# Kernel optimization log

Measured on AMD Instinct MI355X. Metric: run time of the kernel, lower is better.

Reference implementation:

```python
import jax, jax.numpy as jnp
import numpy as np

G = 8          # deformable groups
K = 9          # 3x3 kernel points
MAXR = 10.0    # max_residue_magnitude


def conv2d(x, w, b):
    # x: [B,Cin,H,W], w: [Cout,Cin,3,3], SAME padding, stride 1
    y = jax.lax.conv_general_dilated(x, w, (1, 1), ((1, 1), (1, 1)),
                                     dimension_numbers=('NCHW', 'OIHW', 'NCHW'))
    return y + b[None, :, None, None]


def lrelu(x):
    return jnp.where(x >= 0, x, 0.1 * x)


def offset_branch(x, ws, bs):
    for w, b in zip(ws[:-1], bs[:-1]):
        x = lrelu(conv2d(x, w, b))
    return conv2d(x, ws[-1], bs[-1])


def mdcn(x, offset, mask, w, b):
    # Modulated deformable conv, 3x3, stride 1, pad 1, dilation 1, groups=1.
    # offset: [B, G*K*2, H, W] ordered (g, k, (y,x)); mask: [B, G*K, H, W]
    B, C, H, W = x.shape
    Cg = C // G
    off = offset.reshape(B, G, K, 2, H, W)
    m = mask.reshape(B, G, K, H, W)
    ky = (jnp.arange(K) // 3 - 1).astype(x.dtype)   # kernel dy, pad=1
    kx = (jnp.arange(K) % 3 - 1).astype(x.dtype)    # kernel dx
    hy = jnp.arange(H, dtype=x.dtype)
    wx = jnp.arange(W, dtype=x.dtype)
    py = hy[None, None, None, :, None] + ky[None, None, :, None, None] + off[:, :, :, 0]  # [B,G,K,H,W]
    px = wx[None, None, None, None, :] + kx[None, None, :, None, None] + off[:, :, :, 1]
    y0f = jnp.floor(py); x0f = jnp.floor(px)
    ly = py - y0f; lx = px - x0f
    y0 = y0f.astype(jnp.int32); x0 = x0f.astype(jnp.int32)
    xf = x.reshape(B, G, Cg, H * W)

    def gather(yi, xi):
        valid = ((yi >= 0) & (yi < H) & (xi >= 0) & (xi < W)).astype(x.dtype)
        yc = jnp.clip(yi, 0, H - 1)
        xc = jnp.clip(xi, 0, W - 1)
        idx = (yc * W + xc).reshape(B, G, 1, K * H * W)
        v = jnp.take_along_axis(xf, idx, axis=3).reshape(B, G, Cg, K, H, W)
        return v * valid.reshape(B, G, 1, K, H, W)

    ly_ = ly[:, :, None]; lx_ = lx[:, :, None]  # [B,G,1,K,H,W]
    samp = (gather(y0, x0) * (1 - ly_) * (1 - lx_)
            + gather(y0, x0 + 1) * (1 - ly_) * lx_
            + gather(y0 + 1, x0) * ly_ * (1 - lx_)
            + gather(y0 + 1, x0 + 1) * ly_ * lx_)
    samp = samp * m[:, :, None]                 # modulation
    wr = w.reshape(w.shape[0], G, Cg, K)        # [Cout,G,Cg,K]
    return jnp.einsum('ogck,bgckhw->bohw', wr, samp) + b[None, :, None, None]


def setup_inputs():
    key = jax.random.key(0)
    ks = jax.random.split(key, 40)
    B, C, H, W = 1, 64, 256, 256
    s = 0.05
    inp = {
        'feat_prev': jax.random.normal(ks[0], (B, C, H, W), jnp.float32),
        'feat_next': jax.random.normal(ks[1], (B, C, H, W), jnp.float32),
        'extra_feat_prev': jax.random.normal(ks[2], (B, 2 * C, H, W), jnp.float32),
        'extra_feat_next': jax.random.normal(ks[3], (B, 2 * C, H, W), jnp.float32),
        'flow_prev': jax.random.normal(ks[4], (B, 2, H, W), jnp.float32),
        'flow_next': jax.random.normal(ks[5], (B, 2, H, W), jnp.float32),
    }
    shapes = [(C, 2 * C, 3, 3), (C, C, 3, 3), (C, C, 3, 3), (27 * G, C, 3, 3)]
    i = 6
    for pre in ('off1', 'off2'):
        for j, sh in enumerate(shapes):
            inp[f'{pre}_w{j}'] = jax.random.normal(ks[i], sh, jnp.float32) * s; i += 1
            inp[f'{pre}_b{j}'] = jax.random.normal(ks[i], (sh[0],), jnp.float32) * s; i += 1
    inp['dcn1_w'] = jax.random.normal(ks[i], (C, C, 3, 3), jnp.float32) * s; i += 1
    inp['dcn1_b'] = jax.random.normal(ks[i], (C,), jnp.float32) * s; i += 1
    inp['dcn2_w'] = jax.random.normal(ks[i], (C, C, 3, 3), jnp.float32) * s; i += 1
    inp['dcn2_b'] = jax.random.normal(ks[i], (C,), jnp.float32) * s; i += 1
    inp['fus_w'] = jax.random.normal(ks[i], (C, 2 * C, 3, 3), jnp.float32) * s; i += 1
    inp['fus_b'] = jax.random.normal(ks[i], (C,), jnp.float32) * s
    return inp


def reference(feat_prev, feat_next, extra_feat_prev, extra_feat_next, flow_prev, flow_next,
              off1_w0, off1_b0, off1_w1, off1_b1, off1_w2, off1_b2, off1_w3, off1_b3,
              off2_w0, off2_b0, off2_w1, off2_b1, off2_w2, off2_b2, off2_w3, off2_b3,
              dcn1_w, dcn1_b, dcn2_w, dcn2_b, fus_w, fus_b):
    def branch(feat, extra, flow, ws, bs, dw, db):
        out = offset_branch(extra, ws, bs)
        o1, o2, msk = jnp.split(out, 3, axis=1)
        off = MAXR * jnp.tanh(jnp.concatenate([o1, o2], axis=1))
        off = off + jnp.tile(flow[:, ::-1], (1, off.shape[1] // 2, 1, 1))  # flip(1).repeat
        msk = jax.nn.sigmoid(msk)
        return mdcn(feat, off, msk, dw, db)

    fp = branch(feat_prev, extra_feat_prev, flow_prev,
                [off1_w0, off1_w1, off1_w2, off1_w3], [off1_b0, off1_b1, off1_b2, off1_b3],
                dcn1_w, dcn1_b)
    fn = branch(feat_next, extra_feat_next, flow_next,
                [off2_w0, off2_w1, off2_w2, off2_w3], [off2_b0, off2_b1, off2_b2, off2_b3],
                dcn2_w, dcn2_b)
    return conv2d(jnp.concatenate([fp, fn], axis=1), fus_w, fus_b)
```

## Files before the change

### kernel.cpp

```cpp
#include <hip/hip_runtime.h>
#include <cstddef>
#include <cstdint>

constexpr int IMG = 256;
constexpr int NPIX = 65536;
constexpr int PW = 258;
constexpr size_t PREC = (size_t)PW * PW;

typedef _Float16 h8 __attribute__((ext_vector_type(8)));
typedef float f32x4 __attribute__((ext_vector_type(4)));

template<int CIN>
__device__ __forceinline__ void zero_pad_rec(int i, _Float16* buf)
{
  constexpr int Q = CIN / 8;
  if (i >= 1028 * Q) return;
  int pr = i / Q, qi = i - pr * Q;
  int rec;
  if (pr < 258) rec = pr;
  else if (pr < 516) rec = 257 * 258 + (pr - 258);
  else { int j = pr - 516; rec = (1 + (j >> 1)) * 258 + ((j & 1) ? 257 : 0); }
  *reinterpret_cast<uint4*>(&buf[(size_t)rec * CIN + qi * 8]) = uint4{0, 0, 0, 0};
}

template<int CIN>
__global__ __launch_bounds__(256) void zeropad_k(_Float16* __restrict__ buf)
{
  zero_pad_rec<CIN>(blockIdx.x * 256 + threadIdx.x, buf);
}

template<int CIN>
__global__ __launch_bounds__(256) void prep_hwc_k(
    const float* __restrict__ in, _Float16* __restrict__ out)
{
  int b = blockIdx.x;
  if (b >= 256) { zero_pad_rec<CIN>((b - 256) * 256 + threadIdx.x, out); return; }
  int pix = b * 256 + threadIdx.x;
  int py = pix >> 8, px = pix & 255;
  size_t rec = ((size_t)(py + 1) * PW + px + 1) * CIN;
#pragma unroll
  for (int c0 = 0; c0 < CIN; c0 += 8) {
    _Float16 t[8];
#pragma unroll
    for (int j = 0; j < 8; ++j)
      t[j] = (_Float16)in[(size_t)(c0 + j) * NPIX + pix];
    *reinterpret_cast<uint4*>(&out[rec + c0]) = *reinterpret_cast<uint4*>(t);
  }
}

__device__ __forceinline__ void wfrag(
    const float* __restrict__ w, int cin_tot, int cin_off, int KC, int NBF,
    int nvalid, int idx, _Float16* __restrict__ oHi, _Float16* __restrict__ oLo)
{
  int l = idx & 63;
  int r = idx >> 6;
  int fg = r % NBF; r /= NBF;
  int c = r % KC;
  int t = r / KC;
  int n = fg * 16 + (l & 15);
  int cinb = c * 32 + (l >> 4) * 8;
  _Float16 vh[8], vl[8];
#pragma unroll
  for (int j = 0; j < 8; ++j) {
    float x = 0.f;
    if (n < nvalid) x = w[((size_t)n * cin_tot + cin_off + cinb + j) * 9 + t];
    vh[j] = (_Float16)x;
    vl[j] = (_Float16)(x - (float)vh[j]);
  }
  *reinterpret_cast<uint4*>(oHi + (size_t)idx * 8) = *reinterpret_cast<uint4*>(vh);
  if (oLo)
    *reinterpret_cast<uint4*>(oLo + (size_t)idx * 8) = *reinterpret_cast<uint4*>(vl);
}

__global__ __launch_bounds__(256) void wprep_all_k(
    const float* __restrict__ w0, const float* __restrict__ w1,
    const float* __restrict__ w2, const float* __restrict__ w3,
    const float* __restrict__ wf, int wf_cin_off, const float* __restrict__ dw,
    _Float16* b0h, _Float16* b0l, _Float16* b1h, _Float16* b1l,
    _Float16* b2h, _Float16* b2l, _Float16* b3h, _Float16* b3l,
    _Float16* bfh, _Float16* __restrict__ wB)
{
  int idx = blockIdx.x * 256 + threadIdx.x;
  if (idx < 9216)       wfrag(w0, 128, 0, 4, 4, 64, idx, b0h, b0l);
  else if (idx < 13824) wfrag(w1, 64, 0, 2, 4, 64, idx - 9216, b1h, b1l);
  else if (idx < 18432) wfrag(w2, 64, 0, 2, 4, 64, idx - 13824, b2h, b2l);
  else if (idx < 36864) wfrag(w3, 64, 0, 2, 16, 216, idx - 18432, b3h, b3l);
  else if (idx < 41472) wfrag(wf, 128, wf_cin_off, 2, 4, 64, idx - 36864, bfh, nullptr);
  else if (idx < 46080) {
    int i = idx - 41472;
    int l = i & 63;
    int r = i >> 6;
    int f = r & 3;
    int p = r >> 2;
    int t = p * 4 + (l >> 4);
    int g = (t * 57) >> 9;
    int k = t - 9 * g;
    int n = f * 16 + (l & 15);
    _Float16 v[8];
#pragma unroll
    for (int j = 0; j < 8; ++j)
      v[j] = (_Float16)dw[(size_t)n * 576 + g * 72 + j * 9 + k];
    *reinterpret_cast<uint4*>(wB + (size_t)i * 8) = *reinterpret_cast<uint4*>(v);
  }
}

template<int CIN, int EPI, bool DBL, typename OT>
__global__ __launch_bounds__(256) void conv_mfma_k(
    const _Float16* __restrict__ act, const _Float16* __restrict__ wHi,
    const _Float16* __restrict__ wLo, const float* __restrict__ bias,
    OT* __restrict__ out, int ncout, int NBF)
{
  constexpr int Q = CIN / 8;
  constexpr int KC = CIN / 32;
  constexpr int NT = DBL ? 2 : 1;
  constexpr int NREC = 198;
  __shared__ __align__(16) _Float16 sA[NREC * CIN];

  const int tid = threadIdx.x;
  const int lane = tid & 63;
  const int wv = tid >> 6;
  const int b = blockIdx.x;
  const int inner = b >> 3;
  const int y = (b & 7) * 32 + (inner & 31);
  const int x0 = (inner >> 5) << 6;
  const int n0 = blockIdx.y << 6;

  for (int i = tid; i < NREC * Q; i += 256) {
    int rec = i / Q, q = i - rec * Q;
    int seg = rec / 66, xr = rec - seg * 66;
    size_t g = ((size_t)(y + seg) * PW + x0 + xr) * CIN + q * 8;
    int slot = (q + rec) & (Q - 1);
    *reinterpret_cast<uint4*>(&sA[rec * CIN + slot * 8]) =
        *reinterpret_cast<const uint4*>(&act[g]);
  }

  const int fgb = (n0 >> 4) + wv;
  auto bload = [&](int t, int c, const _Float16* src) {
    return *reinterpret_cast<const h8*>(
        &src[((((size_t)t * KC + c) * NBF + fgb) * 64 + lane) * 8]);
  };
  h8 Bn[KC][NT];
#pragma unroll
  for (int c = 0; c < KC; ++c) {
    Bn[c][0] = bload(0, c, wHi);
    if (DBL) Bn[c][1] = bload(0, c, wLo);
  }

  f32x4 acc[4];
#pragma unroll
  for (int a = 0; a < 4; ++a) acc[a] = f32x4{0.f, 0.f, 0.f, 0.f};
  __syncthreads();

  const int m = lane & 15, kq = lane >> 4;
#pragma unroll 1
  for (int t = 0; t < 9; ++t) {
    h8 Bc[KC][NT];
#pragma unroll
    for (int c = 0; c < KC; ++c) {
      Bc[c][0] = Bn[c][0];
      if (DBL) Bc[c][1] = Bn[c][1];
    }
    if (t < 8) {
#pragma unroll
      for (int c = 0; c < KC; ++c) {
        Bn[c][0] = bload(t + 1, c, wHi);
        if (DBL) Bn[c][1] = bload(t + 1, c, wLo);
      }
    }
    const int lrb = (t / 3) * 66 + (t % 3) + m;
#pragma unroll
    for (int c = 0; c < KC; ++c) {
      const int q = c * 4 + kq;
#pragma unroll
      for (int mf = 0; mf < 4; ++mf) {
        int lr = lrb + mf * 16;
        int slot = (q + lr) & (Q - 1);
        h8 ah = *reinterpret_cast<const h8*>(&sA[lr * CIN + slot * 8]);
        acc[mf] = __builtin_amdgcn_mfma_f32_16x16x32_f16(
            ah, Bc[c][0], acc[mf], 0, 0, 0);
        if (DBL)
          acc[mf] = __builtin_amdgcn_mfma_f32_16x16x32_f16(
              ah, Bc[c][1], acc[mf], 0, 0, 0);
      }
    }
  }

  if (EPI == 0) {
    const int ch = wv * 16 + m;
    const float bv = bias[ch];
#pragma unroll
    for (int mf = 0; mf < 4; ++mf)
#pragma unroll
      for (int r = 0; r < 4; ++r) {
        int p = mf * 16 + kq * 4 + r;
        float v = acc[mf][r] + bv;
        v = (v >= 0.f) ? v : 0.1f * v;
        reinterpret_cast<_Float16*>(out)[((size_t)(y + 1) * PW + x0 + p + 1) * 64 + ch] =
            (_Float16)v;
      }
  } else {
    __syncthreads();
    float* sF = reinterpret_cast<float*>(sA);
    const int nl = wv * 16 + m;
#pragma unroll
    for (int mf = 0; mf < 4; ++mf) {
      int ml = mf * 16 + kq * 4;
      f32x4 v = acc[mf];
      if (EPI == 1) {
        float bv = (n0 + nl < ncout) ? bias[n0 + nl] : 0.f;
        v[0] += bv; v[1] += bv; v[2] += bv; v[3] += bv;
      }
      *reinterpret_cast<f32x4*>(&sF[nl * 68 + ml]) = v;
    }
    __syncthreads();
    for (int i = tid; i < 1024; i += 256) {
      int row = i >> 4, cx = (i & 15) * 4;
      int gc = n0 + row;
      if (gc < ncout) {
        f32x4 v = *reinterpret_cast<f32x4*>(&sF[row * 68 + cx]);
        size_t ob = (size_t)gc * NPIX + (size_t)y * IMG + x0 + cx;
        if (EPI == 2) {
          float* op = reinterpret_cast<float*>(out) + ob;
          op[0] += v[0]; op[1] += v[1]; op[2] += v[2]; op[3] += v[3];
        } else if (sizeof(OT) == 2) {
          _Float16 t4[4] = {(_Float16)v[0], (_Float16)v[1],
                            (_Float16)v[2], (_Float16)v[3]};
          *reinterpret_cast<uint2*>(reinterpret_cast<_Float16*>(out) + ob) =
              *reinterpret_cast<uint2*>(t4);
        } else {
          *reinterpret_cast<f32x4*>(reinterpret_cast<float*>(out) + ob) = v;
        }
      }
    }
  }
}

__global__ __launch_bounds__(256) void featg_k(
    const float* __restrict__ in, _Float16* __restrict__ out)
{
  int pix = blockIdx.x * 256 + threadIdx.x;
#pragma unroll
  for (int g = 0; g < 8; ++g) {
    _Float16 t[8];
#pragma unroll
    for (int c = 0; c < 8; ++c)
      t[c] = (_Float16)in[(size_t)(g * 8 + c) * NPIX + pix];
    *reinterpret_cast<uint4*>(&out[((size_t)g * NPIX + pix) * 8]) =
        *reinterpret_cast<uint4*>(t);
  }
}

struct GS {
  h8 a, b, c, d;
  _Float16 w00, w01, w10, w11;
  float r0, r1, r2;
  h8 bf0, bf1, bf2, bf3;
};

__global__ __launch_bounds__(256, 4) void mdcn_mfma_k(
    const _Float16* __restrict__ featG, const _Float16* __restrict__ o216,
    const float* __restrict__ flow, const _Float16* __restrict__ wB,
    const float* __restrict__ bias, _Float16* __restrict__ actF)
{
  const int tid = threadIdx.x;
  const int lane = tid & 63;
  const int wv = tid >> 6;
  const int b = blockIdx.x;
  const int inner = b >> 3;
  const int row = (b & 7) * 32 + (inner & 31);
  const int xseg = inner >> 5;
  const int m = lane & 15;
  const int tq = lane >> 4;
  const int xw = xseg * 64 + wv * 16;
  const int x = xw + m;
  const int pix = row * 256 + x;

  const float fy = flow[NPIX + pix];
  const float fx = flow[pix];
  const float rowf = (float)row, xf = (float)x;

  f32x4 acc[4];
#pragma unroll
  for (int f = 0; f < 4; ++f) acc[f] = f32x4{0.f, 0.f, 0.f, 0.f};

  auto rawloadv = [&](int p, float& a0, float& a1, float& a2) {
    int t = p * 4 + tq;
    int g = (t * 57) >> 9;
    int k = t - 9 * g;
    a0 = (float)o216[(size_t)(g * 18 + 2 * k) * NPIX + pix];
    a1 = (float)o216[(size_t)(g * 18 + 2 * k + 1) * NPIX + pix];
    a2 = (float)o216[(size_t)(144 + g * 9 + k) * NPIX + pix];
  };

  auto setup = [&](int p, float s0, float s1, float s2, GS& o) {
    const int t = p * 4 + tq;
    const int g = (t * 57) >> 9;
    const int k = t - 9 * g;
    const int kd = (k * 11) >> 5;
    const int km = k - 3 * kd;
    const float mm = __builtin_amdgcn_rcpf(1.f + __expf(-s2));
    const float e0 = __expf(2.f * s0);
    const float e1 = __expf(2.f * s1);
    const float th0 = 1.f - 2.f * __builtin_amdgcn_rcpf(e0 + 1.f);
    const float th1 = 1.f - 2.f * __builtin_amdgcn_rcpf(e1 + 1.f);
    const float pyf = rowf + (float)(kd - 1) + 10.f * th0 + fy;
    const float pxf = xf + (float)(km - 1) + 10.f * th1 + fx;
    const float y0f = floorf(pyf), x0f = floorf(pxf);
    const float ly = pyf - y0f, lx = pxf - x0f;
    const int y0 = (int)y0f, x0i = (int)x0f;
    const int y1 = y0 + 1, x1 = x0i + 1;
    const bool vy0 = (unsigned)y0 < (unsigned)IMG, vy1 = (unsigned)y1 < (unsigned)IMG;
    const bool vx0 = (unsigned)x0i < (unsigned)IMG, vx1 = (unsigned)x1 < (unsigned)IMG;
    const int y0c = min(max(y0, 0), IMG - 1), y1c = min(max(y1, 0), IMG - 1);
    const int x0c = min(max(x0i, 0), IMG - 1), x1c = min(max(x1, 0), IMG - 1);
    const float oy = 1.f - ly, ox = 1.f - lx;
    const float py0 = oy * mm, py1 = ly * mm;
    const float w00 = (vy0 && vx0) ? py0 * ox : 0.f;
    const float w01 = (vy0 && vx1) ? py0 * lx : 0.f;
    const float w10 = (vy1 && vx0) ? py1 * ox : 0.f;
    const float w11 = (vy1 && vx1) ? py1 * lx : 0.f;
    o.w00 = (_Float16)w00; o.w01 = (_Float16)w01;
    o.w10 = (_Float16)w10; o.w11 = (_Float16)w11;
    const _Float16* fg = featG + ((size_t)g << 19);
    o.a = *reinterpret_cast<const h8*>(fg + (size_t)(y0c * IMG + x0c) * 8);
    o.b = *reinterpret_cast<const h8*>(fg + (size_t)(y0c * IMG + x1c) * 8);
    o.c = *reinterpret_cast<const h8*>(fg + (size_t)(y1c * IMG + x0c) * 8);
    o.d = *reinterpret_cast<const h8*>(fg + (size_t)(y1c * IMG + x1c) * 8);
  };

  auto bfload = [&](int p, GS& o) {
    const _Float16* wp = wB + ((size_t)p * 256 + lane) * 8;
    o.bf0 = *reinterpret_cast<const h8*>(wp);
    o.bf1 = *reinterpret_cast<const h8*>(wp + 512);
    o.bf2 = *reinterpret_cast<const h8*>(wp + 1024);
    o.bf3 = *reinterpret_cast<const h8*>(wp + 1536);
  };

  auto consume = [&](GS& cur) {
    h8 af;
#pragma unroll
    for (int j = 0; j < 8; ++j)
      af[j] = (_Float16)(cur.a[j] * cur.w00 + cur.b[j] * cur.w01 +
                         cur.c[j] * cur.w10 + cur.d[j] * cur.w11);
    acc[0] = __builtin_amdgcn_mfma_f32_16x16x32_f16(af, cur.bf0, acc[0], 0, 0, 0);
    acc[1] = __builtin_amdgcn_mfma_f32_16x16x32_f16(af, cur.bf1, acc[1], 0, 0, 0);
    acc[2] = __builtin_amdgcn_mfma_f32_16x16x32_f16(af, cur.bf2, acc[2], 0, 0, 0);
    acc[3] = __builtin_amdgcn_mfma_f32_16x16x32_f16(af, cur.bf3, acc[3], 0, 0, 0);
  };

  auto body = [&](int p, GS& cur, GS& nxt) {
    setup(p + 1, nxt.r0, nxt.r1, nxt.r2, nxt);
    rawloadv(p + 2, cur.r0, cur.r1, cur.r2);
    bfload(p + 1, nxt);
    consume(cur);
  };

  GS A, B;
  {
    float t0, t1, t2;
    rawloadv(0, t0, t1, t2);
    rawloadv(1, B.r0, B.r1, B.r2);
    bfload(0, A);
    setup(0, t0, t1, t2, A);
  }

#pragma unroll 1
  for (int it = 0; it < 8; ++it) {
    body(2 * it, A, B);
    body(2 * it + 1, B, A);
  }
  setup(17, B.r0, B.r1, B.r2, B);
  bfload(17, B);
  consume(A);
  consume(B);

  const size_t rb = ((size_t)(row + 1) * PW + xw + 1) * 64;
#pragma unroll
  for (int f = 0; f < 4; ++f) {
    const int ch = f * 16 + m;
    const float bv = bias[ch];
#pragma unroll
    for (int r = 0; r < 4; ++r)
      actF[rb + (size_t)(tq * 4 + r) * 64 + ch] = (_Float16)(acc[f][r] + bv);
  }
}

extern "C" void kernel_launch(void* const* d_in, const int* in_sizes, int n_in,
                              void* d_out, int out_size, void* d_ws, size_t ws_size,
                              hipStream_t stream)
{
  const float* feat[2]  = {(const float*)d_in[0], (const float*)d_in[1]};
  const float* extra[2] = {(const float*)d_in[2], (const float*)d_in[3]};
  const float* flow[2]  = {(const float*)d_in[4], (const float*)d_in[5]};
  const float* ow[2][4];
  const float* ob[2][4];
  for (int br = 0; br < 2; ++br)
    for (int j = 0; j < 4; ++j) {
      ow[br][j] = (const float*)d_in[6 + br * 8 + j * 2];
      ob[br][j] = (const float*)d_in[6 + br * 8 + j * 2 + 1];
    }
  const float* dcnw[2] = {(const float*)d_in[22], (const float*)d_in[24]};
  const float* dcnb[2] = {(const float*)d_in[23], (const float*)d_in[25]};
  const float* fusw = (const float*)d_in[26];
  const float* fusb = (const float*)d_in[27];

  char* wsb = (char*)d_ws;
  size_t off = 0;
  auto alloc = [&](size_t bytes) {
    void* p = wsb + off;
    off += (bytes + 255) & ~(size_t)255;
    return p;
  };
  _Float16* actI = (_Float16*)alloc(PREC * 128 * 2);
  _Float16* actA = (_Float16*)alloc(PREC * 64 * 2);
  _Float16* actB = (_Float16*)alloc(PREC * 64 * 2);
  _Float16* actF = (_Float16*)alloc(PREC * 64 * 2);
  _Float16* o216 = (_Float16*)alloc((size_t)216 * NPIX * 2);
  _Float16* featG = (_Float16*)alloc((size_t)8 * NPIX * 8 * 2);
  _Float16* wB = (_Float16*)alloc(36864 * 2);
  _Float16* wb0h = (_Float16*)alloc(147456); _Float16* wb0l = (_Float16*)alloc(147456);
  _Float16* wb1h = (_Float16*)alloc(73728);  _Float16* wb1l = (_Float16*)alloc(73728);
  _Float16* wb2h = (_Float16*)alloc(73728);  _Float16* wb2l = (_Float16*)alloc(73728);
  _Float16* wb3h = (_Float16*)alloc(294912); _Float16* wb3l = (_Float16*)alloc(294912);
  _Float16* wbFh = (_Float16*)alloc(73728);
  float* outp = (float*)d_out;

  dim3 blk256(256);
  zeropad_k<64><<<dim3(33), blk256, 0, stream>>>(actA);
  zeropad_k<64><<<dim3(33), blk256, 0, stream>>>(actB);
  zeropad_k<64><<<dim3(33), blk256, 0, stream>>>(actF);

  for (int br = 0; br < 2; ++br) {
    prep_hwc_k<128><<<dim3(321), blk256, 0, stream>>>(extra[br], actI);
    wprep_all_k<<<dim3(180), blk256, 0, stream>>>(
        ow[br][0], ow[br][1], ow[br][2], ow[br][3], fusw, br * 64, dcnw[br],
        wb0h, wb0l, wb1h, wb1l, wb2h, wb2l, wb3h, wb3l, wbFh, wB);

    conv_mfma_k<128, 0, true, _Float16><<<dim3(1024, 1), blk256, 0, stream>>>(
        actI, wb0h, wb0l, ob[br][0], actA, 64, 4);
    conv_mfma_k<64, 0, true, _Float16><<<dim3(1024, 1), blk256, 0, stream>>>(
        actA, wb1h, wb1l, ob[br][1], actB, 64, 4);
    conv_mfma_k<64, 0, true, _Float16><<<dim3(1024, 1), blk256, 0, stream>>>(
        actB, wb2h, wb2l, ob[br][2], actA, 64, 4);
    conv_mfma_k<64, 1, true, _Float16><<<dim3(1024, 4), blk256, 0, stream>>>(
        actA, wb3h, wb3l, ob[br][3], o216, 216, 16);

    featg_k<<<dim3(256), blk256, 0, stream>>>(feat[br], featG);
    mdcn_mfma_k<<<dim3(1024), blk256, 0, stream>>>(
        featG, o216, flow[br], wB, dcnb[br], actF);

    if (br == 0)
      conv_mfma_k<64, 1, false, float><<<dim3(1024, 1), blk256, 0, stream>>>(
          actF, wbFh, nullptr, fusb, outp, 64, 4);
    else
      conv_mfma_k<64, 2, false, float><<<dim3(1024, 1), blk256, 0, stream>>>(
          actF, wbFh, nullptr, nullptr, outp, 64, 4);
  }
}
```

Measured before the change: 515.8 us.

## Batch both branches into single launches and fuse final conv over concatenated channels

Runs the previous and next branches together in every stage by using blockIdx.z to pick per-branch pointers, which halves the launch count and doubles the grid of each kernel. The deformable conv outputs of both branches are written interleaved into one 128-channel padded buffer, so the fusion conv runs once with CIN=128 instead of twice with a read-modify-write accumulate. Workspace buffers are aliased across stages to limit the extra memory. In exchange the working set per kernel doubles, and correctness now depends on the aliasing order and the zero padding of the reused buffers.

```diff
diff --git a/kernel.cpp b/kernel.cpp
--- a/kernel.cpp
+++ b/kernel.cpp
@@ -31,8 +31,12 @@
 
 template<int CIN>
 __global__ __launch_bounds__(256) void prep_hwc_k(
-    const float* __restrict__ in, _Float16* __restrict__ out)
-{
+    const float* __restrict__ in0, const float* __restrict__ in1,
+    _Float16* __restrict__ out0, _Float16* __restrict__ out1)
+{
+  const int z = blockIdx.z;
+  const float* in = z ? in1 : in0;
+  _Float16* out = z ? out1 : out0;
   int b = blockIdx.x;
   if (b >= 256) { zero_pad_rec<CIN>((b - 256) * 256 + threadIdx.x, out); return; }
   int pix = b * 256 + threadIdx.x;
@@ -75,7 +79,7 @@
 __global__ __launch_bounds__(256) void wprep_all_k(
     const float* __restrict__ w0, const float* __restrict__ w1,
     const float* __restrict__ w2, const float* __restrict__ w3,
-    const float* __restrict__ wf, int wf_cin_off, const float* __restrict__ dw,
+    const float* __restrict__ wf, const float* __restrict__ dw,
     _Float16* b0h, _Float16* b0l, _Float16* b1h, _Float16* b1l,
     _Float16* b2h, _Float16* b2l, _Float16* b3h, _Float16* b3l,
     _Float16* bfh, _Float16* __restrict__ wB)
@@ -85,9 +89,8 @@
   else if (idx < 13824) wfrag(w1, 64, 0, 2, 4, 64, idx - 9216, b1h, b1l);
   else if (idx < 18432) wfrag(w2, 64, 0, 2, 4, 64, idx - 13824, b2h, b2l);
   else if (idx < 36864) wfrag(w3, 64, 0, 2, 16, 216, idx - 18432, b3h, b3l);
-  else if (idx < 41472) wfrag(wf, 128, wf_cin_off, 2, 4, 64, idx - 36864, bfh, nullptr);
-  else if (idx < 46080) {
-    int i = idx - 41472;
+  else if (idx < 41472) {
+    int i = idx - 36864;
     int l = i & 63;
     int r = i >> 6;
     int f = r & 3;
@@ -102,19 +105,30 @@
       v[j] = (_Float16)dw[(size_t)n * 576 + g * 72 + j * 9 + k];
     *reinterpret_cast<uint4*>(wB + (size_t)i * 8) = *reinterpret_cast<uint4*>(v);
   }
+  else if (wf && idx < 50688)
+    wfrag(wf, 128, 0, 4, 4, 64, idx - 41472, bfh, nullptr);
 }
 
 template<int CIN, int EPI, bool DBL, typename OT>
 __global__ __launch_bounds__(256) void conv_mfma_k(
-    const _Float16* __restrict__ act, const _Float16* __restrict__ wHi,
-    const _Float16* __restrict__ wLo, const float* __restrict__ bias,
-    OT* __restrict__ out, int ncout, int NBF)
+    const _Float16* __restrict__ act0, const _Float16* __restrict__ act1,
+    const _Float16* __restrict__ wHi0, const _Float16* __restrict__ wHi1,
+    const _Float16* __restrict__ wLo0, const _Float16* __restrict__ wLo1,
+    const float* __restrict__ bias0, const float* __restrict__ bias1,
+    OT* __restrict__ out0, OT* __restrict__ out1, int ncout, int NBF)
 {
   constexpr int Q = CIN / 8;
   constexpr int KC = CIN / 32;
   constexpr int NT = DBL ? 2 : 1;
   constexpr int NREC = 198;
   __shared__ __align__(16) _Float16 sA[NREC * CIN];
+
+  const int z = blockIdx.z;
+  const _Float16* __restrict__ act = z ? act1 : act0;
+  const _Float16* __restrict__ wHi = z ? wHi1 : wHi0;
+  const _Float16* __restrict__ wLo = z ? wLo1 : wLo0;
+  const float* __restrict__ bias = z ? bias1 : bias0;
+  OT* __restrict__ out = z ? out1 : out0;
 
   const int tid = threadIdx.x;
   const int lane = tid & 63;
@@ -206,10 +220,8 @@
     for (int mf = 0; mf < 4; ++mf) {
       int ml = mf * 16 + kq * 4;
       f32x4 v = acc[mf];
-      if (EPI == 1) {
-        float bv = (n0 + nl < ncout) ? bias[n0 + nl] : 0.f;
-        v[0] += bv; v[1] += bv; v[2] += bv; v[3] += bv;
-      }
+      float bv = (n0 + nl < ncout) ? bias[n0 + nl] : 0.f;
+      v[0] += bv; v[1] += bv; v[2] += bv; v[3] += bv;
       *reinterpret_cast<f32x4*>(&sF[nl * 68 + ml]) = v;
     }
     __syncthreads();
@@ -219,10 +231,7 @@
       if (gc < ncout) {
         f32x4 v = *reinterpret_cast<f32x4*>(&sF[row * 68 + cx]);
         size_t ob = (size_t)gc * NPIX + (size_t)y * IMG + x0 + cx;
-        if (EPI == 2) {
-          float* op = reinterpret_cast<float*>(out) + ob;
-          op[0] += v[0]; op[1] += v[1]; op[2] += v[2]; op[3] += v[3];
-        } else if (sizeof(OT) == 2) {
+        if (sizeof(OT) == 2) {
           _Float16 t4[4] = {(_Float16)v[0], (_Float16)v[1],
                             (_Float16)v[2], (_Float16)v[3]};
           *reinterpret_cast<uint2*>(reinterpret_cast<_Float16*>(out) + ob) =
@@ -236,8 +245,12 @@
 }
 
 __global__ __launch_bounds__(256) void featg_k(
-    const float* __restrict__ in, _Float16* __restrict__ out)
-{
+    const float* __restrict__ in0, const float* __restrict__ in1,
+    _Float16* __restrict__ out0, _Float16* __restrict__ out1)
+{
+  const int z = blockIdx.z;
+  const float* in = z ? in1 : in0;
+  _Float16* out = z ? out1 : out0;
   int pix = blockIdx.x * 256 + threadIdx.x;
 #pragma unroll
   for (int g = 0; g < 8; ++g) {
@@ -258,10 +271,21 @@
 };
 
 __global__ __launch_bounds__(256, 4) void mdcn_mfma_k(
-    const _Float16* __restrict__ featG, const _Float16* __restrict__ o216,
-    const float* __restrict__ flow, const _Float16* __restrict__ wB,
-    const float* __restrict__ bias, _Float16* __restrict__ actF)
-{
+    const _Float16* __restrict__ featG0, const _Float16* __restrict__ featG1,
+    const _Float16* __restrict__ o2160, const _Float16* __restrict__ o2161,
+    const float* __restrict__ flow0, const float* __restrict__ flow1,
+    const _Float16* __restrict__ wB0, const _Float16* __restrict__ wB1,
+    const float* __restrict__ bias0, const float* __restrict__ bias1,
+    _Float16* __restrict__ actF)
+{
+  const int z = blockIdx.z;
+  const _Float16* __restrict__ featG = z ? featG1 : featG0;
+  const _Float16* __restrict__ o216 = z ? o2161 : o2160;
+  const float* __restrict__ flow = z ? flow1 : flow0;
+  const _Float16* __restrict__ wB = z ? wB1 : wB0;
+  const float* __restrict__ bias = z ? bias1 : bias0;
+  const int zoff = z << 6;
+
   const int tid = threadIdx.x;
   const int lane = tid & 63;
   const int wv = tid >> 6;
@@ -374,14 +398,14 @@
   consume(A);
   consume(B);
 
-  const size_t rb = ((size_t)(row + 1) * PW + xw + 1) * 64;
+  const size_t rb = ((size_t)(row + 1) * PW + xw + 1) * 128 + zoff;
 #pragma unroll
   for (int f = 0; f < 4; ++f) {
     const int ch = f * 16 + m;
     const float bv = bias[ch];
 #pragma unroll
     for (int r = 0; r < 4; ++r)
-      actF[rb + (size_t)(tq * 4 + r) * 64 + ch] = (_Float16)(acc[f][r] + bv);
+      actF[rb + (size_t)(tq * 4 + r) * 128 + ch] = (_Float16)(acc[f][r] + bv);
   }
 }
 
@@ -411,49 +435,71 @@
     off += (bytes + 255) & ~(size_t)255;
     return p;
   };
-  _Float16* actI = (_Float16*)alloc(PREC * 128 * 2);
-  _Float16* actA = (_Float16*)alloc(PREC * 64 * 2);
-  _Float16* actB = (_Float16*)alloc(PREC * 64 * 2);
-  _Float16* actF = (_Float16*)alloc(PREC * 64 * 2);
-  _Float16* o216 = (_Float16*)alloc((size_t)216 * NPIX * 2);
-  _Float16* featG = (_Float16*)alloc((size_t)8 * NPIX * 8 * 2);
-  _Float16* wB = (_Float16*)alloc(36864 * 2);
-  _Float16* wb0h = (_Float16*)alloc(147456); _Float16* wb0l = (_Float16*)alloc(147456);
-  _Float16* wb1h = (_Float16*)alloc(73728);  _Float16* wb1l = (_Float16*)alloc(73728);
-  _Float16* wb2h = (_Float16*)alloc(73728);  _Float16* wb2l = (_Float16*)alloc(73728);
-  _Float16* wb3h = (_Float16*)alloc(294912); _Float16* wb3l = (_Float16*)alloc(294912);
-  _Float16* wbFh = (_Float16*)alloc(73728);
+  _Float16* R1 = (_Float16*)alloc(PREC * 128 * 2 * 2);
+  _Float16* actI0 = R1;
+  _Float16* actI1 = R1 + PREC * 128;
+  _Float16* actB0 = R1;
+  _Float16* actB1 = R1 + PREC * 64;
+  _Float16* actF  = R1;
+  _Float16* R2 = (_Float16*)alloc(PREC * 64 * 2 * 2);
+  _Float16* actA0 = R2;
+  _Float16* actA1 = R2 + PREC * 64;
+  _Float16* featG0 = R2;
+  _Float16* featG1 = R2 + PREC * 64;
+  _Float16* o2160 = (_Float16*)alloc((size_t)216 * NPIX * 2 * 2);
+  _Float16* o2161 = o2160 + (size_t)216 * NPIX;
+  _Float16* wB0 = (_Float16*)alloc(73728 * 2);
+  _Float16* wB1 = wB0 + 36864;
+  _Float16* wb0h[2] = {(_Float16*)alloc(147456), (_Float16*)alloc(147456)};
+  _Float16* wb0l[2] = {(_Float16*)alloc(147456), (_Float16*)alloc(147456)};
+  _Float16* wb1h[2] = {(_Float16*)alloc(73728), (_Float16*)alloc(73728)};
+  _Float16* wb1l[2] = {(_Float16*)alloc(73728), (_Float16*)alloc(73728)};
+  _Float16* wb2h[2] = {(_Float16*)alloc(73728), (_Float16*)alloc(73728)};
+  _Float16* wb2l[2] = {(_Float16*)alloc(73728), (_Float16*)alloc(73728)};
+  _Float16* wb3h[2] = {(_Float16*)alloc(294912), (_Float16*)alloc(294912)};
+  _Float16* wb3l[2] = {(_Float16*)alloc(294912), (_Float16*)alloc(294912)};
+  _Float16* wbFh = (_Float16*)alloc(147456);
   float* outp = (float*)d_out;
 
   dim3 blk256(256);
-  zeropad_k<64><<<dim3(33), blk256, 0, stream>>>(actA);
-  zeropad_k<64><<<dim3(33), blk256, 0, stream>>>(actB);
-  zeropad_k<64><<<dim3(33), blk256, 0, stream>>>(actF);
-
-  for (int br = 0; br < 2; ++br) {
-    prep_hwc_k<128><<<dim3(321), blk256, 0, stream>>>(extra[br], actI);
-    wprep_all_k<<<dim3(180), blk256, 0, stream>>>(
-        ow[br][0], ow[br][1], ow[br][2], ow[br][3], fusw, br * 64, dcnw[br],
-        wb0h, wb0l, wb1h, wb1l, wb2h, wb2l, wb3h, wb3l, wbFh, wB);
-
-    conv_mfma_k<128, 0, true, _Float16><<<dim3(1024, 1), blk256, 0, stream>>>(
-        actI, wb0h, wb0l, ob[br][0], actA, 64, 4);
-    conv_mfma_k<64, 0, true, _Float16><<<dim3(1024, 1), blk256, 0, stream>>>(
-        actA, wb1h, wb1l, ob[br][1], actB, 64, 4);
-    conv_mfma_k<64, 0, true, _Float16><<<dim3(1024, 1), blk256, 0, stream>>>(
-        actB, wb2h, wb2l, ob[br][2], actA, 64, 4);
-    conv_mfma_k<64, 1, true, _Float16><<<dim3(1024, 4), blk256, 0, stream>>>(
-        actA, wb3h, wb3l, ob[br][3], o216, 216, 16);
-
-    featg_k<<<dim3(256), blk256, 0, stream>>>(feat[br], featG);
-    mdcn_mfma_k<<<dim3(1024), blk256, 0, stream>>>(
-        featG, o216, flow[br], wB, dcnb[br], actF);
-
-    if (br == 0)
-      conv_mfma_k<64, 1, false, float><<<dim3(1024, 1), blk256, 0, stream>>>(
-          actF, wbFh, nullptr, fusb, outp, 64, 4);
-    else
-      conv_mfma_k<64, 2, false, float><<<dim3(1024, 1), blk256, 0, stream>>>(
-          actF, wbFh, nullptr, nullptr, outp, 64, 4);
-  }
-}
+  zeropad_k<64><<<dim3(33), blk256, 0, stream>>>(actA0);
+  zeropad_k<64><<<dim3(33), blk256, 0, stream>>>(actA1);
+
+  wprep_all_k<<<dim3(198), blk256, 0, stream>>>(
+      ow[0][0], ow[0][1], ow[0][2], ow[0][3], fusw, dcnw[0],
+      wb0h[0], wb0l[0], wb1h[0], wb1l[0], wb2h[0], wb2l[0],
+      wb3h[0], wb3l[0], wbFh, wB0);
+  wprep_all_k<<<dim3(162), blk256, 0, stream>>>(
+      ow[1][0], ow[1][1], ow[1][2], ow[1][3], nullptr, dcnw[1],
+      wb0h[1], wb0l[1], wb1h[1], wb1l[1], wb2h[1], wb2l[1],
+      wb3h[1], wb3l[1], nullptr, wB1);
+
+  prep_hwc_k<128><<<dim3(321, 1, 2), blk256, 0, stream>>>(
+      extra[0], extra[1], actI0, actI1);
+
+  conv_mfma_k<128, 0, true, _Float16><<<dim3(1024, 1, 2), blk256, 0, stream>>>(
+      actI0, actI1, wb0h[0], wb0h[1], wb0l[0], wb0l[1],
+      ob[0][0], ob[1][0], actA0, actA1, 64, 4);
+  zeropad_k<64><<<dim3(33), blk256, 0, stream>>>(actB0);
+  zeropad_k<64><<<dim3(33), blk256, 0, stream>>>(actB1);
+  conv_mfma_k<64, 0, true, _Float16><<<dim3(1024, 1, 2), blk256, 0, stream>>>(
+      actA0, actA1, wb1h[0], wb1h[1], wb1l[0], wb1l[1],
+      ob[0][1], ob[1][1], actB0, actB1, 64, 4);
+  conv_mfma_k<64, 0, true, _Float16><<<dim3(1024, 1, 2), blk256, 0, stream>>>(
+      actB0, actB1, wb2h[0], wb2h[1], wb2l[0], wb2l[1],
+      ob[0][2], ob[1][2], actA0, actA1, 64, 4);
+  zeropad_k<128><<<dim3(65), blk256, 0, stream>>>(actF);
+  conv_mfma_k<64, 1, true, _Float16><<<dim3(1024, 4, 2), blk256, 0, stream>>>(
+      actA0, actA1, wb3h[0], wb3h[1], wb3l[0], wb3l[1],
+      ob[0][3], ob[1][3], o2160, o2161, 216, 16);
+
+  featg_k<<<dim3(256, 1, 2), blk256, 0, stream>>>(
+      feat[0], feat[1], featG0, featG1);
+  mdcn_mfma_k<<<dim3(1024, 1, 2), blk256, 0, stream>>>(
+      featG0, featG1, o2160, o2161, flow[0], flow[1],
+      wB0, wB1, dcnb[0], dcnb[1], actF);
+
+  conv_mfma_k<128, 1, false, float><<<dim3(1024, 1, 1), blk256, 0, stream>>>(
+      actF, actF, wbFh, wbFh, nullptr, nullptr,
+      fusb, fusb, outp, outp, 64, 4);
+}
```

Result: no change. 516.4 us (+0.1%).
